# Optimization experiments

Hardware: AMD Instinct MI355X
Metric: run time of the kernel (lower is better)

The kernel has to match this reference:

```python
import jax, jax.numpy as jnp
import numpy as np

N = 10000      # nodes
E = 160000     # edges (before self-loops)
IN = 256
NEG_SLOPE = 0.2  # PyG GATConv default


def gat_layer(x, src, dst, W, a_src, a_dst, bias, heads, concat, n):
    # x: [n, in_dim]; W: [in_dim, heads*C]; a_src/a_dst: [heads, C]
    C = W.shape[1] // heads
    h = (x @ W).reshape(n, heads, C)                      # [n,H,C]
    es = jnp.einsum('nhc,hc->nh', h, a_src)               # [n,H]
    ed = jnp.einsum('nhc,hc->nh', h, a_dst)               # [n,H]
    e = jax.nn.leaky_relu(es[src] + ed[dst], NEG_SLOPE)   # [E,H]
    # segment softmax over destination node (every node has a self-loop)
    emax = jax.ops.segment_max(e, dst, num_segments=n)    # [n,H]
    al = jnp.exp(e - emax[dst])                           # [E,H]
    den = jax.ops.segment_sum(al, dst, num_segments=n)    # [n,H]
    al = al / den[dst]
    out = jax.ops.segment_sum(h[src] * al[:, :, None], dst, num_segments=n)  # [n,H,C]
    out = out.reshape(n, heads * C) if concat else out.mean(axis=1)
    return out + bias


def setup_inputs() -> dict:
    key = jax.random.key(0)
    ks = jax.random.split(key, 16)
    s = 0.05
    p = lambda k, shp: jax.random.normal(k, shp, dtype=jnp.float32) * s
    return {
        'x': jax.random.normal(ks[0], (N, IN), dtype=jnp.float32),
        'edge_index': jax.random.randint(ks[1], (2, E), 0, N, dtype=jnp.int64),
        'proj_w': p(ks[2], (IN, 512)), 'proj_b': jnp.zeros((512,), jnp.float32),
        'w1': p(ks[3], (512, 4 * 512)),  'as1': p(ks[4], (4, 512)), 'ad1': p(ks[5], (4, 512)),  'b1': jnp.zeros((2048,), jnp.float32),
        'w2': p(ks[6], (2048, 4 * 512)), 'as2': p(ks[7], (4, 512)), 'ad2': p(ks[8], (4, 512)),  'b2': jnp.zeros((2048,), jnp.float32),
        'w3': p(ks[9], (2048, 2 * 512)), 'as3': p(ks[10], (2, 512)), 'ad3': p(ks[11], (2, 512)), 'b3': jnp.zeros((512,), jnp.float32),
    }


def reference(x, edge_index, proj_w, proj_b, w1, as1, ad1, b1,
              w2, as2, ad2, b2, w3, as3, ad3, b3):
    n = x.shape[0]
    loops = jnp.arange(n, dtype=edge_index.dtype)
    src = jnp.concatenate([edge_index[0], loops])   # PyG add_self_loops=True
    dst = jnp.concatenate([edge_index[1], loops])
    h = x @ proj_w + proj_b                         # dropout is identity in eval
    h = gat_layer(h, src, dst, w1, as1, ad1, b1, 4, True, n)
    h = jax.nn.elu(h)
    h = gat_layer(h, src, dst, w2, as2, ad2, b2, 4, True, n)
    h = jax.nn.elu(h)
    h = gat_layer(h, src, dst, w3, as3, ad3, b3, 2, False, n)
    return h
```

## Files before the change

### kernel.cpp

```cpp
#include <hip/hip_runtime.h>
#include <hip/hip_bf16.h>
#include <math.h>

#define CDIV(a,b) (((a)+(b)-1)/(b))

typedef __bf16  bf16x8 __attribute__((ext_vector_type(8)));
typedef float   f32x4  __attribute__((ext_vector_type(4)));
typedef unsigned short u16x8 __attribute__((ext_vector_type(8)));
typedef unsigned short u16x4 __attribute__((ext_vector_type(4)));

__device__ __forceinline__ float bf2f(unsigned short u) {
    union { unsigned int i; float f; } x; x.i = ((unsigned int)u) << 16; return x.f;
}
__device__ __forceinline__ unsigned short f2bf(float f) {
    union { float f; unsigned int i; } x; x.f = f;
    unsigned int r = x.i + 0x7fff + ((x.i >> 16) & 1);
    return (unsigned short)(r >> 16);
}

__global__ void hist_kernel(const int* __restrict__ ei, int* __restrict__ deg,
                            int E, int Et) {
    int e = blockIdx.x * blockDim.x + threadIdx.x;
    if (e >= Et) return;
    int d = (e < E) ? ei[E + e] : (e - E);
    atomicAdd(&deg[d], 1);
}

__global__ void scan_kernel(const int* __restrict__ deg, int* __restrict__ off, int n) {
    __shared__ int wsum[16];
    __shared__ int carry_s;
    int t = threadIdx.x, lane = t & 63, wv = t >> 6;
    if (t == 0) carry_s = 0;
    __syncthreads();
    for (int base = 0; base < n; base += 1024) {
        int v = (base + t < n) ? deg[base + t] : 0;
        int x = v;
#pragma unroll
        for (int o = 1; o < 64; o <<= 1) {
            int y = __shfl_up(x, o);
            if (lane >= o) x += y;
        }
        if (lane == 63) wsum[wv] = x;
        __syncthreads();
        if (wv == 0 && lane < 16) {
            int s = wsum[lane];
#pragma unroll
            for (int o = 1; o < 16; o <<= 1) {
                int y = __shfl_up(s, o);
                if (lane >= o) s += y;
            }
            wsum[lane] = s;
        }
        __syncthreads();
        int wprev = (wv == 0) ? 0 : wsum[wv - 1];
        int incl = carry_s + wprev + x;
        if (base + t < n) off[base + t] = incl - v;
        __syncthreads();
        if (t == 1023) carry_s = incl;
        __syncthreads();
    }
    if (t == 0) off[n] = carry_s;
}

__global__ void scatter_kernel(const int* __restrict__ ei, const int* __restrict__ off,
                               int* __restrict__ cur, int* __restrict__ csr,
                               int E, int Et) {
    int e = blockIdx.x * blockDim.x + threadIdx.x;
    if (e >= Et) return;
    int s, d;
    if (e < E) { s = ei[e]; d = ei[E + e]; } else { s = e - E; d = s; }
    int pos = off[d] + atomicAdd(&cur[d], 1);
    csr[pos] = s;
}

__global__ void prep_t_kernel(const float* __restrict__ wa, __hip_bfloat16* __restrict__ wta,
                              const float* __restrict__ wb, __hip_bfloat16* __restrict__ wtb,
                              const float* __restrict__ wc, __hip_bfloat16* __restrict__ wtc,
                              int t0, int t1, int t2) {
    __shared__ float tile[32][33];
    int bid = blockIdx.x;
    const float* w; __hip_bfloat16* wt; int K, N, r;
    if (bid < t0)      { w = wa; wt = wta; K = 512;  N = 2048; r = bid; }
    else if (bid < t1) { w = wb; wt = wtb; K = 2048; N = 2048; r = bid - t0; }
    else               { w = wc; wt = wtc; K = 2048; N = 1024; r = bid - t1; }
    (void)t2;
    int kt = K >> 5;
    int kb = (r % kt) * 32, nb = (r / kt) * 32;
    int tx = threadIdx.x & 31, ty = threadIdx.x >> 5;
    for (int i = ty; i < 32; i += 8)
        tile[i][tx] = w[(size_t)(kb + i) * N + nb + tx];
    __syncthreads();
    for (int i = ty; i < 32; i += 8)
        wt[(size_t)(nb + i) * K + kb + tx] = __float2bfloat16(tile[tx][i]);
}

__global__ void cvt2_kernel(const float* __restrict__ a, __hip_bfloat16* __restrict__ ao,
                            int na4,
                            const float* __restrict__ b, __hip_bfloat16* __restrict__ bo,
                            int nb4) {
    int i = blockIdx.x * blockDim.x + threadIdx.x;
    const float* src; __hip_bfloat16* dst; int idx;
    if (i < na4) { src = a; dst = ao; idx = i * 4; }
    else if (i < na4 + nb4) { src = b; dst = bo; idx = (i - na4) * 4; }
    else return;
    float4 v = *(const float4*)(src + idx);
    dst[idx + 0] = __float2bfloat16(v.x);
    dst[idx + 1] = __float2bfloat16(v.y);
    dst[idx + 2] = __float2bfloat16(v.z);
    dst[idx + 3] = __float2bfloat16(v.w);
}

__global__ void beff_kernel(const float* __restrict__ pb, const float* __restrict__ w1,
                            float* __restrict__ beff, int N) {
    int j  = blockIdx.x * 256 + threadIdx.x;
    int k0 = blockIdx.y * 64;
    float s = 0.f;
#pragma unroll
    for (int k = 0; k < 64; k++)
        s = fmaf(pb[k0 + k], w1[(size_t)(k0 + k) * N + j], s);
    atomicAdd(&beff[j], s);
}

__global__ void va_kernel(const __hip_bfloat16* __restrict__ w_efft,
                          const float* __restrict__ b_eff,
                          const float* __restrict__ as1, const float* __restrict__ ad1,
                          const float* __restrict__ b1,
                          float* __restrict__ va, float* __restrict__ cvec,
                          float* __restrict__ b1s) {
    int j = blockIdx.x, t = threadIdx.x;
    if (j == 8) {
        for (int i = t; i < 2048; i += 256) b1s[i] = b_eff[i] + b1[i];
        return;
    }
    int h = j & 3;
    const float* a = ((j < 4) ? as1 : ad1) + h * 512;
    __shared__ float aLDS[512];
    __shared__ float red[256];
    for (int c = t; c < 512; c += 256) aLDS[c] = a[c];
    __syncthreads();
    float acc = 0.f;
    const unsigned short* wb = (const unsigned short*)w_efft + (size_t)h * 512 * 256 + t;
    for (int c = 0; c < 512; c++)
        acc = fmaf(aLDS[c], bf2f(wb[(size_t)c * 256]), acc);
    va[j * 256 + t] = acc;
    float cp = b_eff[h * 512 + t] * aLDS[t] + b_eff[h * 512 + 256 + t] * aLDS[256 + t];
    red[t] = cp;
    __syncthreads();
    for (int s = 128; s > 0; s >>= 1) {
        if (t < s) red[t] += red[t + s];
        __syncthreads();
    }
    if (t == 0) cvec[j] = red[0];
}

__global__ void es1_kernel(const __hip_bfloat16* __restrict__ x_bf,
                           const float* __restrict__ va, const float* __restrict__ cvec,
                           float* __restrict__ es, float* __restrict__ ed) {
    int node = blockIdx.x, l = threadIdx.x;
    u16x4 xv = *(const u16x4*)((const unsigned short*)x_bf + (size_t)node * 256 + l * 4);
    float xf[4];
#pragma unroll
    for (int k = 0; k < 4; k++) xf[k] = bf2f(xv[k]);
    float dot[8];
#pragma unroll
    for (int j = 0; j < 8; j++) {
        float4 v = *(const float4*)(va + j * 256 + l * 4);
        dot[j] = xf[0] * v.x + xf[1] * v.y + xf[2] * v.z + xf[3] * v.w;
    }
#pragma unroll
    for (int j = 0; j < 8; j++)
        for (int o = 32; o; o >>= 1) dot[j] += __shfl_down(dot[j], o);
    if (l == 0) {
#pragma unroll
        for (int h = 0; h < 4; h++) {
            es[node * 4 + h] = dot[h] + cvec[h];
            ed[node * 4 + h] = dot[4 + h] + cvec[4 + h];
        }
    }
}

__global__ __launch_bounds__(256) void agg1x_kernel(
    const __hip_bfloat16* __restrict__ x_bf, const float* __restrict__ es,
    const float* __restrict__ ed, const int* __restrict__ csr,
    const int* __restrict__ off, __hip_bfloat16* __restrict__ z)
{
    __shared__ float alds[64][4];
    __shared__ int   slds[64];
    int d = blockIdx.x, t = threadIdx.x;
    int beg = off[d], end = off[d + 1];
    float acc[4] = {0.f, 0.f, 0.f, 0.f}, den[4] = {0.f, 0.f, 0.f, 0.f};
    float edd[4];
#pragma unroll
    for (int h = 0; h < 4; h++) edd[h] = ed[d * 4 + h];
    const unsigned short* xb = (const unsigned short*)x_bf;

    for (int cb = beg; cb < end; cb += 64) {
        int cl = end - cb; if (cl > 64) cl = 64;
        int i = t >> 2, h = t & 3;
        if (i < cl) {
            int s = csr[cb + i];
            if (h == 0) slds[i] = s;
            float e = es[s * 4 + h] + edd[h];
            e = (e > 0.f) ? e : 0.2f * e;
            alds[i][h] = __expf(e);
        }
        __syncthreads();
        for (int ii = 0; ii < cl; ii++) {
            int s = slds[ii];
            float xv = bf2f(xb[(size_t)s * 256 + t]);
#pragma unroll
            for (int hh = 0; hh < 4; hh++) {
                float a = alds[ii][hh];
                den[hh] += a;
                acc[hh] = fmaf(a, xv, acc[hh]);
            }
        }
        __syncthreads();
    }
    unsigned short* zb = (unsigned short*)z + (size_t)d * 1024;
#pragma unroll
    for (int h = 0; h < 4; h++)
        zb[h * 256 + t] = f2bf(acc[h] / den[h]);
}

__device__ __forceinline__ void gload16(void* lds, const void* g) {
    __builtin_amdgcn_global_load_lds(
        (const __attribute__((address_space(1))) void*)g,
        (__attribute__((address_space(3))) void*)lds, 16, 0, 0);
}

__global__ __launch_bounds__(256) void gemm_bf16_kernel(
    const __hip_bfloat16* __restrict__ A,
    const __hip_bfloat16* __restrict__ BT,
    const float* __restrict__ bias,
    __hip_bfloat16* __restrict__ Cb,
    int M, int N, int K, int lda, int hko, int do_elu,
    int MB, int NB, int XT, int NBH)
{
    __shared__ __align__(16) __hip_bfloat16 As[128 * 32];
    __shared__ __align__(16) __hip_bfloat16 Bs[128 * 32];

    const int bid  = blockIdx.x;
    const int xcd  = bid & 7;
    const int slot = bid >> 3;
    const int per_yh = XT * NBH;
    const int yh    = slot / per_yh;
    const int rem   = slot - yh * per_yh;
    const int x_sub = rem / NBH;
    const int ys    = rem - x_sub * NBH;
    const int yb    = yh * NBH + ys;
    const int xb    = xcd * XT + x_sub;
    if (xb >= MB || yb >= NB) return;

    const int tid = threadIdx.x;
    const int m0 = xb * 128, n0 = yb * 128;
    const int w = tid >> 6, l = tid & 63;
    const int wm = (w & 1) * 64, wn = (w >> 1) * 64;
    const int lm = l & 15, lq = l >> 4;

    f32x4 acc[4][4] = {};

    const int arow = tid >> 2;
    const int acol = (tid & 3) * 8;
    const __hip_bfloat16* Ag = A + (size_t)(m0 + arow) * lda + acol + (n0 >> 9) * hko;
    const __hip_bfloat16* Bg = BT + (size_t)(n0 + arow) * K + acol;
    char* AsW = (char*)As + (w << 10);
    char* BsW = (char*)Bs + (w << 10);

    for (int k0 = 0; k0 < K; k0 += 32) {
        gload16(AsW,        Ag + k0);
        gload16(AsW + 4096, Ag + (size_t)64 * lda + k0);
        gload16(BsW,        Bg + k0);
        gload16(BsW + 4096, Bg + (size_t)64 * K + k0);
        __syncthreads();
        bf16x8 af[4], bfr[4];
#pragma unroll
        for (int i = 0; i < 4; i++)
            af[i] = *(const bf16x8*)(As + (wm + i * 16 + lm) * 32 + lq * 8);
#pragma unroll
        for (int j = 0; j < 4; j++)
            bfr[j] = *(const bf16x8*)(Bs + (wn + j * 16 + lm) * 32 + lq * 8);
#pragma unroll
        for (int i = 0; i < 4; i++)
#pragma unroll
            for (int j = 0; j < 4; j++)
                acc[i][j] = __builtin_amdgcn_mfma_f32_16x16x32_bf16(
                    af[i], bfr[j], acc[i][j], 0, 0, 0);
        __syncthreads();
    }

#pragma unroll
    for (int i = 0; i < 4; i++) {
        int rb = m0 + wm + i * 16 + lq * 4;
#pragma unroll
        for (int r = 0; r < 4; r++) {
            int row = rb + r;
            if (row >= M) continue;
#pragma unroll
            for (int j = 0; j < 4; j++) {
                int col = n0 + wn + j * 16 + lm;
                float v = acc[i][j][r];
                if (bias) v += bias[col];
                if (do_elu) v = (v > 0.f) ? v : expm1f(v);
                Cb[(size_t)row * N + col] = __float2bfloat16(v);
            }
        }
    }
}

__global__ __launch_bounds__(512, 2) void gemm256_kernel(
    const __hip_bfloat16* __restrict__ A,
    const __hip_bfloat16* __restrict__ BT,
    __hip_bfloat16* __restrict__ Cb,
    int M, int N, int K, int MT)
{
    __shared__ __align__(16) char smem[131072];
    const int NT = K >> 6;

    const int cpx  = gridDim.x >> 3;
    const int bid  = blockIdx.x;
    const int slot = (bid & 7) * cpx + (bid >> 3);
    const int mt   = slot % MT, ntl = slot / MT;
    const int m0 = mt << 8, n0 = ntl << 8;

    const int tid = threadIdx.x;
    const int w  = tid >> 6, l = tid & 63;
    const int wr = w >> 2, wc = w & 3;
    const int lm = l & 15, lq = l >> 4;

    const int srow = tid >> 3;
    const int scol = ((l & 7) << 3) ^ ((l >> 3) << 3);
    const __hip_bfloat16* As0 = A  + (size_t)(m0 + srow) * K + scol;
    const __hip_bfloat16* Bs0 = BT + (size_t)(n0 + srow) * K + scol;
    const size_t rs64  = (size_t)64  * K;
    const size_t rs128 = (size_t)128 * K;
    char* const stA = smem +          ((size_t)w << 10);
    char* const stB = smem + 65536 +  ((size_t)w << 10);

    auto STAGE_A = [&](int par, int hf, int tt) {
        char* d = stA + (((par << 1) | hf) << 14);
        const __hip_bfloat16* s = As0 + (size_t)hf * rs128 + (tt << 6);
        gload16(d,        s);
        gload16(d + 8192, s + rs64);
    };
    auto STAGE_B = [&](int par, int hf, int tt) {
        char* d = stB + (((par << 1) | hf) << 14);
        const __hip_bfloat16* s = Bs0 + (size_t)hf * rs128 + (tt << 6);
        gload16(d,        s);
        gload16(d + 8192, s + rs64);
    };

    const int roff = lm << 7;
    const int xm   = (lm & 7) << 4;
    const int off0 = (lq << 4) ^ xm;
    const int off1 = off0 ^ 64;
    const int bsel = 65536 + ((wc & 1) << 13);

    f32x4  acc[8][4] = {};
    bf16x8 af[8][2];
    bf16x8 bfr[2][2];

    STAGE_A(0, 0, 0); STAGE_A(0, 1, 0);
    STAGE_B(0, 0, 0); STAGE_B(0, 1, 0);
    STAGE_A(1, 0, 1); STAGE_A(1, 1, 1);
    asm volatile("s_waitcnt vmcnt(4)" ::: "memory");
    __builtin_amdgcn_s_barrier();

    for (int t = 0; t < NT; ++t) {
        const int par = t & 1;
        const char* aS = smem + (((par << 1) | wr)        << 14) + roff;
        const char* bS = smem + (((par << 1) | (wc >> 1)) << 14) + bsel + roff;

#pragma unroll
        for (int i = 0; i < 4; ++i) {
            af[i][0] = *(const bf16x8*)(aS + i * 2048 + off0);
            af[i][1] = *(const bf16x8*)(aS + i * 2048 + off1);
        }
#pragma unroll
        for (int j = 0; j < 2; ++j) {
            bfr[j][0] = *(const bf16x8*)(bS + j * 2048 + off0);
            bfr[j][1] = *(const bf16x8*)(bS + j * 2048 + off1);
        }
        if (t + 1 < NT) STAGE_B(par ^ 1, 0, t + 1);
        __builtin_amdgcn_s_barrier();
        asm volatile("s_waitcnt lgkmcnt(0)" ::: "memory");
        __builtin_amdgcn_sched_barrier(0);
        __builtin_amdgcn_s_setprio(1);
#pragma unroll
        for (int i = 0; i < 4; ++i)
#pragma unroll
            for (int j = 0; j < 2; ++j) {
                acc[i][j] = __builtin_amdgcn_mfma_f32_16x16x32_bf16(af[i][0], bfr[j][0], acc[i][j], 0, 0, 0);
                acc[i][j] = __builtin_amdgcn_mfma_f32_16x16x32_bf16(af[i][1], bfr[j][1], acc[i][j], 0, 0, 0);
            }
        __builtin_amdgcn_s_setprio(0);
        __builtin_amdgcn_s_barrier();

#pragma unroll
        for (int i = 4; i < 8; ++i) {
            af[i][0] = *(const bf16x8*)(aS + i * 2048 + off0);
            af[i][1] = *(const bf16x8*)(aS + i * 2048 + off1);
        }
        if (t + 1 < NT) STAGE_B(par ^ 1, 1, t + 1);
        __builtin_amdgcn_s_barrier();
        asm volatile("s_waitcnt lgkmcnt(0)" ::: "memory");
        __builtin_amdgcn_sched_barrier(0);
        __builtin_amdgcn_s_setprio(1);
#pragma unroll
        for (int i = 4; i < 8; ++i)
#pragma unroll
            for (int j = 0; j < 2; ++j) {
                acc[i][j] = __builtin_amdgcn_mfma_f32_16x16x32_bf16(af[i][0], bfr[j][0], acc[i][j], 0, 0, 0);
                acc[i][j] = __builtin_amdgcn_mfma_f32_16x16x32_bf16(af[i][1], bfr[j][1], acc[i][j], 0, 0, 0);
            }
        __builtin_amdgcn_s_setprio(0);
        __builtin_amdgcn_s_barrier();

#pragma unroll
        for (int j = 0; j < 2; ++j) {
            bfr[j][0] = *(const bf16x8*)(bS + (j + 2) * 2048 + off0);
            bfr[j][1] = *(const bf16x8*)(bS + (j + 2) * 2048 + off1);
        }
        if (t + 2 < NT) STAGE_A(par, 0, t + 2);
        __builtin_amdgcn_s_barrier();
        asm volatile("s_waitcnt lgkmcnt(0)" ::: "memory");
        __builtin_amdgcn_sched_barrier(0);
        __builtin_amdgcn_s_setprio(1);
#pragma unroll
        for (int i = 0; i < 4; ++i)
#pragma unroll
            for (int j = 0; j < 2; ++j) {
                acc[i][j + 2] = __builtin_amdgcn_mfma_f32_16x16x32_bf16(af[i][0], bfr[j][0], acc[i][j + 2], 0, 0, 0);
                acc[i][j + 2] = __builtin_amdgcn_mfma_f32_16x16x32_bf16(af[i][1], bfr[j][1], acc[i][j + 2], 0, 0, 0);
            }
        __builtin_amdgcn_s_setprio(0);
        __builtin_amdgcn_s_barrier();

        if (t + 2 < NT) STAGE_A(par, 1, t + 2);
        __builtin_amdgcn_s_barrier();
        __builtin_amdgcn_sched_barrier(0);
        __builtin_amdgcn_s_setprio(1);
#pragma unroll
        for (int i = 4; i < 8; ++i)
#pragma unroll
            for (int j = 0; j < 2; ++j) {
                acc[i][j + 2] = __builtin_amdgcn_mfma_f32_16x16x32_bf16(af[i][0], bfr[j][0], acc[i][j + 2], 0, 0, 0);
                acc[i][j + 2] = __builtin_amdgcn_mfma_f32_16x16x32_bf16(af[i][1], bfr[j][1], acc[i][j + 2], 0, 0, 0);
            }
        __builtin_amdgcn_s_setprio(0);
        if (t + 2 < NT)      { asm volatile("s_waitcnt vmcnt(4)" ::: "memory"); }
        else if (t + 1 < NT) { asm volatile("s_waitcnt vmcnt(0)" ::: "memory"); }
        __builtin_amdgcn_s_barrier();
    }

#pragma unroll
    for (int i = 0; i < 8; ++i) {
        int rb = m0 + wr * 128 + i * 16 + lq * 4;
#pragma unroll
        for (int r = 0; r < 4; ++r) {
            int row = rb + r;
            if (row >= M) continue;
#pragma unroll
            for (int j = 0; j < 4; ++j) {
                int col = n0 + wc * 64 + j * 16 + lm;
                Cb[(size_t)row * N + col] = __float2bfloat16(acc[i][j][r]);
            }
        }
    }
}

__global__ void esed_kernel(const __hip_bfloat16* __restrict__ h,
                            const float* __restrict__ a_src,
                            const float* __restrict__ a_dst,
                            float* __restrict__ es, float* __restrict__ ed, int H) {
    int nidx = blockIdx.x;
    int t = threadIdx.x;
    int head = t >> 6, lane = t & 63;
    const unsigned short* hp =
        (const unsigned short*)h + (size_t)nidx * H * 512 + head * 512 + lane * 8;
    const float* sp = a_src + head * 512 + lane * 8;
    const float* dp = a_dst + head * 512 + lane * 8;
    u16x8 hv = *(const u16x8*)hp;
    float4 s0 = *(const float4*)sp, s1 = *(const float4*)(sp + 4);
    float4 d0 = *(const float4*)dp, d1 = *(const float4*)(dp + 4);
    float hf[8];
#pragma unroll
    for (int k = 0; k < 8; k++) hf[k] = bf2f(hv[k]);
    float s = hf[0]*s0.x + hf[1]*s0.y + hf[2]*s0.z + hf[3]*s0.w
            + hf[4]*s1.x + hf[5]*s1.y + hf[6]*s1.z + hf[7]*s1.w;
    float d = hf[0]*d0.x + hf[1]*d0.y + hf[2]*d0.z + hf[3]*d0.w
            + hf[4]*d1.x + hf[5]*d1.y + hf[6]*d1.z + hf[7]*d1.w;
    for (int o = 32; o; o >>= 1) { s += __shfl_down(s, o); d += __shfl_down(d, o); }
    if (lane == 0) { es[nidx * H + head] = s; ed[nidx * H + head] = d; }
}

template<int H, int VEC, bool MEAN>
__global__ __launch_bounds__(256) void agg_kernel(
    const __hip_bfloat16* __restrict__ h, const float* __restrict__ es,
    const float* __restrict__ ed, const int* __restrict__ csr,
    const int* __restrict__ off, const float* __restrict__ bias,
    float* __restrict__ outF, __hip_bfloat16* __restrict__ outB, int do_elu)
{
    constexpr int HS = H * 512;
    __shared__ float red[MEAN ? 1024 : 1];
    int d = blockIdx.x, t = threadIdx.x;
    int c0 = t * VEC;
    int head = c0 >> 9;
    float edd = ed[d * H + head];
    int beg = off[d], end = off[d + 1];
    float acc[VEC];
#pragma unroll
    for (int k = 0; k < VEC; k++) acc[k] = 0.f;
    float den = 0.f;
    const unsigned short* hb = (const unsigned short*)h;

    int i = beg;
    for (; i + 3 < end; i += 4) {
        int   s[4];
        float wgt[4];
#pragma unroll
        for (int u = 0; u < 4; u++) {
            s[u] = csr[i + u];
            float e = es[s[u] * H + head] + edd;
            e = (e > 0.f) ? e : 0.2f * e;
            wgt[u] = __expf(e);
        }
        if constexpr (VEC == 8) {
            u16x8 v[4];
#pragma unroll
            for (int u = 0; u < 4; u++)
                v[u] = *(const u16x8*)(hb + (size_t)s[u] * HS + c0);
#pragma unroll
            for (int u = 0; u < 4; u++) {
                den += wgt[u];
#pragma unroll
                for (int k = 0; k < 8; k++) acc[k] = fmaf(wgt[u], bf2f(v[u][k]), acc[k]);
            }
        } else {
            u16x4 v[4];
#pragma unroll
            for (int u = 0; u < 4; u++)
                v[u] = *(const u16x4*)(hb + (size_t)s[u] * HS + c0);
#pragma unroll
            for (int u = 0; u < 4; u++) {
                den += wgt[u];
#pragma unroll
                for (int k = 0; k < VEC; k++) acc[k] = fmaf(wgt[u], bf2f(v[u][k]), acc[k]);
            }
        }
    }
    for (; i < end; i++) {
        int s0 = csr[i];
        float e0 = es[s0 * H + head] + edd;
        e0 = (e0 > 0.f) ? e0 : 0.2f * e0;
        float w0 = __expf(e0);
        den += w0;
        const unsigned short* hp0 = hb + (size_t)s0 * HS + c0;
        if constexpr (VEC == 8) {
            u16x8 v0 = *(const u16x8*)hp0;
#pragma unroll
            for (int k = 0; k < 8; k++) acc[k] = fmaf(w0, bf2f(v0[k]), acc[k]);
        } else {
            u16x4 v0 = *(const u16x4*)hp0;
#pragma unroll
            for (int k = 0; k < VEC; k++) acc[k] = fmaf(w0, bf2f(v0[k]), acc[k]);
        }
    }

    float inv = 1.f / den;
    if constexpr (!MEAN) {
        u16x8 ov;
#pragma unroll
        for (int k = 0; k < VEC; k++) {
            float v = acc[k] * inv + bias[c0 + k];
            if (do_elu) v = (v > 0.f) ? v : expm1f(v);
            ov[k] = f2bf(v);
        }
        *(u16x8*)((unsigned short*)outB + (size_t)d * HS + c0) = ov;
    } else {
#pragma unroll
        for (int k = 0; k < VEC; k++) red[c0 + k] = acc[k] * inv;
        __syncthreads();
        if (t < 128) {
#pragma unroll
            for (int k = 0; k < 4; k++) {
                int c = t * 4 + k;
                outF[(size_t)d * 512 + c] = 0.5f * (red[c] + red[c + 512]) + bias[c];
            }
        }
    }
}

extern "C" void kernel_launch(void* const* d_in, const int* in_sizes, int n_in,
                              void* d_out, int out_size, void* d_ws, size_t ws_size,
                              hipStream_t stream) {
    const float* x      = (const float*)d_in[0];
    const int*   ei     = (const int*)  d_in[1];
    const float* proj_w = (const float*)d_in[2];
    const float* proj_b = (const float*)d_in[3];
    const float* w1  = (const float*)d_in[4];
    const float* as1 = (const float*)d_in[5];
    const float* ad1 = (const float*)d_in[6];
    const float* b1  = (const float*)d_in[7];
    const float* w2  = (const float*)d_in[8];
    const float* as2 = (const float*)d_in[9];
    const float* ad2 = (const float*)d_in[10];
    const float* b2  = (const float*)d_in[11];
    const float* w3  = (const float*)d_in[12];
    const float* as3 = (const float*)d_in[13];
    const float* ad3 = (const float*)d_in[14];
    const float* b3  = (const float*)d_in[15];

    const int n    = in_sizes[0] / 256;
    const int E    = in_sizes[1] / 2;
    const int Et   = E + n;
    const int MB   = CDIV(n, 128);
    const int MB2  = CDIV(n, 256);
    const int Mpad = MB2 * 256;
    const int XT   = CDIV(MB, 8);

    char* p = (char*)d_ws;
    auto carve = [&](size_t bytes) {
        void* r = (void*)p;
        p += (bytes + 255) & ~(size_t)255;
        return r;
    };
    __hip_bfloat16* h_bf    = (__hip_bfloat16*)carve((size_t)Mpad * 2048 * sizeof(__hip_bfloat16));
    __hip_bfloat16* act_bf  = (__hip_bfloat16*)carve((size_t)Mpad * 2048 * sizeof(__hip_bfloat16));
    __hip_bfloat16* x_bf    = (__hip_bfloat16*)carve((size_t)Mpad * 256 * sizeof(__hip_bfloat16));
    __hip_bfloat16* pw_bf   = (__hip_bfloat16*)carve((size_t)256 * 512 * sizeof(__hip_bfloat16));
    __hip_bfloat16* w1t     = (__hip_bfloat16*)carve((size_t)2048 * 512 * sizeof(__hip_bfloat16));
    __hip_bfloat16* w2t     = (__hip_bfloat16*)carve((size_t)2048 * 2048 * sizeof(__hip_bfloat16));
    __hip_bfloat16* w3t     = (__hip_bfloat16*)carve((size_t)1024 * 2048 * sizeof(__hip_bfloat16));
    __hip_bfloat16* w_efft  = (__hip_bfloat16*)carve((size_t)2048 * 256 * sizeof(__hip_bfloat16));
    float* b_eff = (float*)carve((size_t)2048 * sizeof(float));
    float* b1s   = (float*)carve((size_t)2048 * sizeof(float));
    float* va    = (float*)carve((size_t)8 * 256 * sizeof(float));
    float* cvec  = (float*)carve((size_t)8 * sizeof(float));
    float* es  = (float*)carve((size_t)n * 4 * sizeof(float));
    float* ed  = (float*)carve((size_t)n * 4 * sizeof(float));
    int* deg = (int*)carve((size_t)2 * n * sizeof(int));
    int* cur = deg + n;
    int* off = (int*)carve((size_t)(n + 1) * sizeof(int));
    int* csr = (int*)carve((size_t)Et * sizeof(int));
    __hip_bfloat16* z_bf = h_bf;
    (void)ws_size; (void)n_in;

    hipMemsetAsync(deg, 0, 2 * n * sizeof(int), stream);
    hipMemsetAsync(b_eff, 0, 2048 * sizeof(float), stream);
    hist_kernel<<<CDIV(Et, 256), 256, 0, stream>>>(ei, deg, E, Et);
    scan_kernel<<<1, 1024, 0, stream>>>(deg, off, n);
    scatter_kernel<<<CDIV(Et, 256), 256, 0, stream>>>(ei, off, cur, csr, E, Et);

    const int t0 = (512 / 32) * (2048 / 32);
    const int t1 = t0 + (2048 / 32) * (2048 / 32);
    const int t2 = t1 + (2048 / 32) * (1024 / 32);
    prep_t_kernel<<<t2, 256, 0, stream>>>(w1, w1t, w2, w2t, w3, w3t, t0, t1, t2);
    const int na4 = 256 * 512 / 4, nb4 = n * 256 / 4;
    cvt2_kernel<<<CDIV(na4 + nb4, 256), 256, 0, stream>>>(proj_w, pw_bf, na4, x, x_bf, nb4);

    gemm_bf16_kernel<<<8 * 2 * 2, 256, 0, stream>>>(
        w1t, pw_bf, nullptr, w_efft, 2048, 256, 512, 512, 0, 0, 16, 2, 2, 2);
    beff_kernel<<<dim3(2048 / 256, 512 / 64), 256, 0, stream>>>(proj_b, w1, b_eff, 2048);

    va_kernel<<<9, 256, 0, stream>>>(w_efft, b_eff, as1, ad1, b1, va, cvec, b1s);

    auto gemm_grid = [&](int NB) { return 8 * XT * NB; };

    es1_kernel<<<n, 64, 0, stream>>>(x_bf, va, cvec, es, ed);
    agg1x_kernel<<<n, 256, 0, stream>>>(x_bf, es, ed, csr, off, z_bf);
    gemm_bf16_kernel<<<gemm_grid(16), 256, 0, stream>>>(
        z_bf, w_efft, b1s, act_bf, n, 2048, 256, 1024, 256, 1, MB, 16, XT, 16);

    gemm256_kernel<<<8 * MB2, 512, 0, stream>>>(act_bf, w2t, h_bf, n, 2048, 2048, MB2);
    esed_kernel<<<n, 4 * 64, 0, stream>>>(h_bf, as2, ad2, es, ed, 4);
    agg_kernel<4, 8, false><<<n, 256, 0, stream>>>(h_bf, es, ed, csr, off, b2,
                                                   nullptr, act_bf, 1);

    gemm256_kernel<<<4 * MB2, 512, 0, stream>>>(act_bf, w3t, h_bf, n, 1024, 2048, MB2);
    esed_kernel<<<n, 2 * 64, 0, stream>>>(h_bf, as3, ad3, es, ed, 2);
    agg_kernel<2, 4, true><<<n, 256, 0, stream>>>(h_bf, es, ed, csr, off, b3,
                                                  (float*)d_out, nullptr, 0);
}
```

Measured before the change: 619.5 us.

## Split layer-2 GEMM into 256 and 128 tiles and use 128-tile GEMM for layer 3

Adds a 128x128-tile double-buffered MFMA GEMM kernel. The layer-2 GEMM is now split into two launches: 256x256 tiles cover most of the output with exactly 256 blocks, and a second launch of 128x128 tiles covers the leftover region (last column tiles and the tail rows). Layer 3 moves entirely to 128x128 tiles with 640 blocks. The aim is to cut wave-quantization tail waste on the 256 compute units, at the cost of hardcoded tile-mapping constants that assume n=10000 and an extra kernel launch.

Measured after the change: 602.7 us. 2.7% less time.

```diff
diff --git a/kernel.cpp b/kernel.cpp
--- a/kernel.cpp
+++ b/kernel.cpp
@@ -312,7 +312,7 @@
     const __hip_bfloat16* __restrict__ A,
     const __hip_bfloat16* __restrict__ BT,
     __hip_bfloat16* __restrict__ Cb,
-    int M, int N, int K, int MT)
+    int M, int N, int K, int MT, int nfull)
 {
     __shared__ __align__(16) char smem[131072];
     const int NT = K >> 6;
@@ -320,7 +320,9 @@
     const int cpx  = gridDim.x >> 3;
     const int bid  = blockIdx.x;
     const int slot = (bid & 7) * cpx + (bid >> 3);
-    const int mt   = slot % MT, ntl = slot / MT;
+    int mt, ntl;
+    if (slot < nfull) { mt = slot % MT; ntl = slot / MT; }
+    else              { ntl = nfull / MT; mt = (nfull % MT) + (slot - nfull); }
     const int m0 = mt << 8, n0 = ntl << 8;
 
     const int tid = threadIdx.x;
@@ -464,6 +466,105 @@
             for (int j = 0; j < 4; ++j) {
                 int col = n0 + wc * 64 + j * 16 + lm;
                 Cb[(size_t)row * N + col] = __float2bfloat16(acc[i][j][r]);
+            }
+        }
+    }
+}
+
+__global__ __launch_bounds__(256, 2) void gemm128_kernel(
+    const __hip_bfloat16* __restrict__ A,
+    const __hip_bfloat16* __restrict__ BT,
+    __hip_bfloat16* __restrict__ Cb,
+    int M, int N, int K, int mode, int RT)
+{
+    __shared__ __align__(16) char smem[65536];
+    const int NT = K >> 6;
+
+    const int cpx  = gridDim.x >> 3;
+    const int bid  = blockIdx.x;
+    const int slot = (bid & 7) * cpx + (bid >> 3);
+    int r, c;
+    if (mode == 0) { r = slot % RT; c = slot / RT; }
+    else {
+        if (slot < 96) { c = 12 + slot / 48; r = 32 + slot % 48; }
+        else           { int u = slot - 96; c = 14 + u / 80; r = u % 80; }
+    }
+    const int m0 = r << 7, n0 = c << 7;
+
+    const int tid = threadIdx.x;
+    const int w = tid >> 6, l = tid & 63;
+    const int wm = (w & 1) << 6, wn = (w >> 1) << 6;
+    const int lm = l & 15, lq = l >> 4;
+
+    const int srow = tid >> 3;
+    const int scol = (((tid & 7) ^ ((tid >> 3) & 7)) << 3);
+    const __hip_bfloat16* Ag = A  + (size_t)(m0 + srow) * K + scol;
+    const __hip_bfloat16* Bg = BT + (size_t)(n0 + srow) * K + scol;
+    const size_t rs32 = (size_t)32 * K;
+    char* const dA = smem +         ((size_t)w << 10);
+    char* const dB = smem + 16384 + ((size_t)w << 10);
+
+    auto STAGE = [&](int par, int tt) {
+        char* pa = dA + (par << 15);
+        char* pb = dB + (par << 15);
+        const __hip_bfloat16* sa = Ag + (tt << 6);
+        const __hip_bfloat16* sb = Bg + (tt << 6);
+#pragma unroll
+        for (int s = 0; s < 4; ++s) {
+            gload16(pa + (s << 12), sa + (size_t)s * rs32);
+            gload16(pb + (s << 12), sb + (size_t)s * rs32);
+        }
+    };
+
+    const int roff = lm << 7;
+    const int off0 = (lq << 4) ^ ((lm & 7) << 4);
+    const int off1 = off0 ^ 64;
+
+    f32x4 acc[4][4] = {};
+
+    STAGE(0, 0);
+    asm volatile("s_waitcnt vmcnt(0)" ::: "memory");
+    __builtin_amdgcn_s_barrier();
+
+    for (int t = 0; t < NT; ++t) {
+        const int par = t & 1;
+        if (t + 1 < NT) STAGE(par ^ 1, t + 1);
+        const char* aS = smem + (par << 15) +         wm * 128 + roff;
+        const char* bS = smem + (par << 15) + 16384 + wn * 128 + roff;
+        bf16x8 af[4][2], bfr[4][2];
+#pragma unroll
+        for (int i = 0; i < 4; ++i) {
+            af[i][0]  = *(const bf16x8*)(aS + i * 2048 + off0);
+            af[i][1]  = *(const bf16x8*)(aS + i * 2048 + off1);
+            bfr[i][0] = *(const bf16x8*)(bS + i * 2048 + off0);
+            bfr[i][1] = *(const bf16x8*)(bS + i * 2048 + off1);
+        }
+        asm volatile("s_waitcnt lgkmcnt(0)" ::: "memory");
+        __builtin_amdgcn_sched_barrier(0);
+        __builtin_amdgcn_s_setprio(1);
+#pragma unroll
+        for (int i = 0; i < 4; ++i)
+#pragma unroll
+            for (int j = 0; j < 4; ++j) {
+                acc[i][j] = __builtin_amdgcn_mfma_f32_16x16x32_bf16(af[i][0], bfr[j][0], acc[i][j], 0, 0, 0);
+                acc[i][j] = __builtin_amdgcn_mfma_f32_16x16x32_bf16(af[i][1], bfr[j][1], acc[i][j], 0, 0, 0);
+            }
+        __builtin_amdgcn_s_setprio(0);
+        if (t + 1 < NT) asm volatile("s_waitcnt vmcnt(0)" ::: "memory");
+        __builtin_amdgcn_s_barrier();
+    }
+
+#pragma unroll
+    for (int i = 0; i < 4; ++i) {
+        int rb = m0 + wm + i * 16 + lq * 4;
+#pragma unroll
+        for (int r2 = 0; r2 < 4; ++r2) {
+            int row = rb + r2;
+            if (row >= M) continue;
+#pragma unroll
+            for (int j = 0; j < 4; ++j) {
+                int col = n0 + wn + j * 16 + lm;
+                Cb[(size_t)row * N + col] = __float2bfloat16(acc[i][j][r2]);
             }
         }
     }
@@ -665,19 +766,18 @@
 
     va_kernel<<<9, 256, 0, stream>>>(w_efft, b_eff, as1, ad1, b1, va, cvec, b1s);
 
-    auto gemm_grid = [&](int NB) { return 8 * XT * NB; };
-
     es1_kernel<<<n, 64, 0, stream>>>(x_bf, va, cvec, es, ed);
     agg1x_kernel<<<n, 256, 0, stream>>>(x_bf, es, ed, csr, off, z_bf);
-    gemm_bf16_kernel<<<gemm_grid(16), 256, 0, stream>>>(
+    gemm_bf16_kernel<<<8 * XT * 16, 256, 0, stream>>>(
         z_bf, w_efft, b1s, act_bf, n, 2048, 256, 1024, 256, 1, MB, 16, XT, 16);
 
-    gemm256_kernel<<<8 * MB2, 512, 0, stream>>>(act_bf, w2t, h_bf, n, 2048, 2048, MB2);
+    gemm256_kernel<<<256, 512, 0, stream>>>(act_bf, w2t, h_bf, n, 2048, 2048, 40, 240);
+    gemm128_kernel<<<256, 256, 0, stream>>>(act_bf, w2t, h_bf, n, 2048, 2048, 1, 0);
     esed_kernel<<<n, 4 * 64, 0, stream>>>(h_bf, as2, ad2, es, ed, 4);
     agg_kernel<4, 8, false><<<n, 256, 0, stream>>>(h_bf, es, ed, csr, off, b2,
                                                    nullptr, act_bf, 1);
 
-    gemm256_kernel<<<4 * MB2, 512, 0, stream>>>(act_bf, w3t, h_bf, n, 1024, 2048, MB2);
+    gemm128_kernel<<<640, 256, 0, stream>>>(act_bf, w3t, h_bf, n, 1024, 2048, 0, 80);
     esed_kernel<<<n, 2 * 64, 0, stream>>>(h_bf, as3, ad3, es, ed, 2);
     agg_kernel<2, 4, true><<<n, 256, 0, stream>>>(h_bf, es, ed, csr, off, b3,
                                                   (float*)d_out, nullptr, 0);
```
